# Kernel tuning notes

Measured on AMD Instinct MI355X. Metric: run time of the kernel, lower is better.

The kernel has to match this reference:

```python
import jax, jax.numpy as jnp
import numpy as np

NEG_INF = jnp.float32(-1e30)


def setup_inputs() -> dict:
    key = jax.random.key(0)
    k1, k2, k3, k4 = jax.random.split(key, 4)
    B, L1, L2, H = 64, 1024, 1024, 128
    x = jax.random.normal(k1, (B, L1, H), dtype=jnp.float32)
    y = jax.random.normal(k2, (B, L2, H), dtype=jnp.float32)
    y_mask = jax.random.uniform(k3, (B, L2)) < 0.2
    W = jax.random.normal(k4, (H, H), dtype=jnp.float32) * (1.0 / np.sqrt(H))
    b = jnp.zeros((H,), dtype=jnp.float32)
    return {"x": x, "y": y, "y_mask": y_mask, "W": W, "b": b}


def reference(x, y, y_mask, W, b):
    # shared linear + relu projections (torch Linear: x @ W.T + b)
    x_proj = jax.nn.relu(jnp.einsum("bld,hd->blh", x, W) + b)  # [B, L1, H]
    y_proj = jax.nn.relu(jnp.einsum("bld,hd->blh", y, W) + b)  # [B, L2, H]
    # unscaled cross-attention scores
    scores = jnp.einsum("bih,bjh->bij", x_proj, y_proj)  # [B, L1, L2]
    scores = jnp.where(y_mask[:, None, :], NEG_INF, scores)
    alpha = jax.nn.softmax(scores, axis=-1)  # [B, L1, L2]
    # weighted sum over original (unprojected) y
    matched_seq = jnp.einsum("bij,bjh->bih", alpha, y)  # [B, L1, H]
    return matched_seq
```

## Files before the change

### kernel.cpp

```cpp
#include <hip/hip_runtime.h>
#include <hip/hip_bf16.h>


typedef __attribute__((ext_vector_type(8))) short    s8v;
typedef __attribute__((ext_vector_type(8))) _Float16 h8v;
typedef __attribute__((ext_vector_type(4))) _Float16 h4v;
typedef __attribute__((ext_vector_type(4))) float    f4v;

#define BDIM 256

__device__ __forceinline__ f4v mfma_bf16(s8v a, s8v b, f4v c) {
    return __builtin_amdgcn_mfma_f32_16x16x32_bf16(a, b, c, 0, 0, 0);
}
__device__ __forceinline__ f4v mfma_f16(h8v a, h8v b, f4v c) {
    return __builtin_amdgcn_mfma_f32_16x16x32_f16(a, b, c, 0, 0, 0);
}
__device__ __forceinline__ void tsplit(float v, short& hi, short& lo) {
    unsigned b = __builtin_bit_cast(unsigned, v);
    unsigned hb = b & 0xFFFF0000u;
    float res = v - __builtin_bit_cast(float, hb);
    hi = (short)(hb >> 16);
    lo = (short)(__builtin_bit_cast(unsigned, res) >> 16);
}

typedef const __attribute__((address_space(1))) unsigned int gu32;
typedef __attribute__((address_space(3))) unsigned int lu32;
__device__ __forceinline__ void gld_lds16(const void* g, void* l) {
    __builtin_amdgcn_global_load_lds((gu32*)g, (lu32*)l, 16, 0, 0);
}

__global__ __launch_bounds__(1024) void prep_kernel(
    const unsigned int* __restrict__ mraw, unsigned char* __restrict__ nm,
    const float* __restrict__ W, short* __restrict__ Whsw, short* __restrict__ Wlsw)
{
    if (blockIdx.x == 1) {
        for (int idx = threadIdx.x; idx < 16384; idx += 1024) {
            int r = idx >> 7, c = idx & 127;
            short hi, lo; tsplit(W[idx], hi, lo);
            int cs = (((c >> 3) ^ (r & 15)) << 3) | (c & 7);
            Whsw[r * 128 + cs] = hi;
            Wlsw[r * 128 + cs] = lo;
        }
        return;
    }
    __shared__ unsigned int sOrAll, sOrOdd;
    if (threadIdx.x == 0) { sOrAll = 0u; sOrOdd = 0u; }
    __syncthreads();
    unsigned int oa = 0u, oo = 0u;
    for (int i = threadIdx.x; i < 16384; i += 1024) {
        unsigned int v = mraw[i];
        oa |= v;
        if (i & 1) oo |= v;
    }
    atomicOr(&sOrAll, oa);
    atomicOr(&sOrOdd, oo);
    __syncthreads();
    const unsigned int orv = sOrAll, oro = sOrOdd;
    int mode;
    if (orv <= 1u)                       mode = (orv == 1u && oro == 0u) ? 3 : 0;
    else if ((orv & 0xFEFEFEFEu) == 0u)  mode = 1;
    else if ((orv & 0x0000FFFFu) == 0u)  mode = 0;
    else                                 mode = 2;
    const unsigned char*  b8  = (const unsigned char*)mraw;
    const unsigned short* b16 = (const unsigned short*)mraw;
    for (int j = threadIdx.x; j < 65536; j += 1024) {
        unsigned int v;
        if (mode == 0)      v = mraw[j];
        else if (mode == 1) v = b8[j];
        else if (mode == 2) v = b16[j];
        else                v = mraw[2 * j] | mraw[2 * j + 1];
        nm[j] = v ? 1 : 0;
    }
}

__global__ __launch_bounds__(BDIM, 4) void proj_kernel(
    const float* __restrict__ X, const float* __restrict__ Y,
    const short* __restrict__ Whsw, const short* __restrict__ Wlsw,
    const float* __restrict__ bias,
    _Float16* __restrict__ XPf, _Float16* __restrict__ YPsw,
    _Float16* __restrict__ YTsw)
{
    __shared__ short sW[2][64][128];

    const int gid = blockIdx.x;
    const float* src; int local;
    if (gid < 1024) { src = X; local = gid; }
    else            { src = Y; local = gid - 1024; }
    const int row0 = (local >> 1) * 128, h0 = (local & 1) * 64;
    const int t = threadIdx.x, w = t >> 6, lane = t & 63, c = lane & 15, q = lane >> 4;

    {
        const short* g0 = Whsw + h0 * 128;
        const short* g1 = Wlsw + h0 * 128;
        short* l0 = &sW[0][0][0];
        short* l1 = &sW[1][0][0];
        for (int i = 0; i < 4; ++i) {
            int off = (t + i * BDIM) * 8;
            *(s8v*)(l0 + off) = *(const s8v*)(g0 + off);
            *(s8v*)(l1 + off) = *(const s8v*)(g1 + off);
        }
    }

    f4v rawA[2][4], rawB[2][4];
#pragma unroll
    for (int set = 0; set < 2; ++set) {
        const float* xr = src + (size_t)(row0 + w * 32 + set * 16 + c) * 128;
#pragma unroll
        for (int ks = 0; ks < 4; ++ks) {
            rawA[set][ks] = *(const f4v*)&xr[ks * 32 + q * 8];
            rawB[set][ks] = *(const f4v*)&xr[ks * 32 + q * 8 + 4];
        }
    }
    __syncthreads();

    f4v zero = {0.f, 0.f, 0.f, 0.f};
#pragma unroll
    for (int set = 0; set < 2; ++set) {
        s8v ah[4], al[4];
#pragma unroll
        for (int ks = 0; ks < 4; ++ks) {
            for (int k = 0; k < 4; ++k) {
                short hh, ll;
                tsplit(rawA[set][ks][k], hh, ll); ah[ks][k] = hh;     al[ks][k] = ll;
                tsplit(rawB[set][ks][k], hh, ll); ah[ks][4 + k] = hh; al[ks][4 + k] = ll;
            }
        }
        f4v acc[4];
        for (int n = 0; n < 4; ++n) acc[n] = zero;
#pragma unroll
        for (int ks = 0; ks < 4; ++ks) {
            s8v bh[4], bl[4];
            for (int nt = 0; nt < 4; ++nt) {
                int cs = (((ks * 4 + q) ^ c) << 3);
                bh[nt] = *(const s8v*)&sW[0][nt * 16 + c][cs];
                bl[nt] = *(const s8v*)&sW[1][nt * 16 + c][cs];
            }
            for (int nt = 0; nt < 4; ++nt) {
                acc[nt] = mfma_bf16(ah[ks], bh[nt], acc[nt]);
                acc[nt] = mfma_bf16(al[ks], bh[nt], acc[nt]);
                acc[nt] = mfma_bf16(ah[ks], bl[nt], acc[nt]);
            }
        }
        for (int nt = 0; nt < 4; ++nt) {
            float bv = bias[h0 + nt * 16 + c];
            for (int r = 0; r < 4; ++r) {
                float v = fmaxf(acc[nt][r] + bv, 0.0f);
                int grow = row0 + w * 32 + set * 16 + q * 4 + r;
                int h = h0 + nt * 16 + c;
                if (gid < 1024) {
                    XPf[(size_t)grow * 128 + h] = (_Float16)v;
                } else {
                    int jt = (grow >> 6) & 15, jr = grow & 63;
                    int chunk = (h >> 3) ^ (jr & 7);
                    size_t off = (size_t)((grow >> 10) * 16 + jt) * 8192
                                 + jr * 128 + chunk * 8 + (h & 7);
                    YPsw[off] = (_Float16)v;
                }
            }
        }
    }

    if (gid >= 1024 && h0 == 0) {
        __syncthreads();
        _Float16* sT = (_Float16*)&sW[0][0][0];
#pragma unroll
        for (int set = 0; set < 2; ++set) {
            int row = w * 32 + set * 16 + c;
            int tile = row >> 6, j6 = row & 63;
            int jlo = j6 & 7, jhb = (j6 >> 3);
#pragma unroll
            for (int ks = 0; ks < 4; ++ks) {
                for (int k = 0; k < 4; ++k) {
                    int h = ks * 32 + q * 8 + k;
                    sT[tile * 8192 + h * 64 + (((jhb ^ (h & 7)) << 3) | jlo)] =
                        (_Float16)rawA[set][ks][k];
                    int h2 = h + 4;
                    sT[tile * 8192 + h2 * 64 + (((jhb ^ (h2 & 7)) << 3) | jlo)] =
                        (_Float16)rawB[set][ks][k];
                }
            }
        }
        __syncthreads();
        _Float16* dst = YTsw + (size_t)(row0 >> 6) * 8192;
        for (int i = 0; i < 8; ++i) {
            int idx = t + i * BDIM;
            *(h8v*)(dst + idx * 8) = *(const h8v*)(sT + idx * 8);
        }
    }
}

__global__ __launch_bounds__(512, 4) void attn_kernel(
    const _Float16* __restrict__ YPsw, const _Float16* __restrict__ YTsw,
    const unsigned char* __restrict__ nmask,
    const _Float16* __restrict__ XPf, float* __restrict__ out)
{
    __shared__ _Float16 sTile[2][16384];
    __shared__ _Float16 sP[128 * 64];

    const int id = blockIdx.x;
    const int xcd = id & 7, rest = id >> 3;
    const int ibase = (rest & 7) * 128;
    const int b = xcd + 8 * (rest >> 3);
    const int t = threadIdx.x, wave = t >> 6, lane = t & 63;
    const int c = lane & 15, q = lane >> 4;
    const int mrow = b * 1024;

    h8v afrag[4];
    {
        const _Float16* xr = XPf + (size_t)(mrow + ibase + wave * 16 + c) * 128;
        for (int ks = 0; ks < 4; ++ks)
            afrag[ks] = *(const h8v*)&xr[ks * 32 + q * 8];
    }

    const char* gYP = (const char*)(YPsw + (size_t)b * 16 * 8192);
    const char* gYT = (const char*)(YTsw + (size_t)b * 16 * 8192);
    const int soff = wave * 1024 + lane * 16;

    {
        char* lp = (char*)&sTile[0][0]    + wave * 1024;
        char* lt = (char*)&sTile[0][8192] + wave * 1024;
        for (int i = 0; i < 2; ++i) {
            gld_lds16(gYP + soff + i * 8192, lp + i * 8192);
            gld_lds16(gYT + soff + i * 8192, lt + i * 8192);
        }
    }

    unsigned mw[4];
    for (int nt = 0; nt < 4; ++nt)
        mw[nt] = *(const unsigned*)(nmask + mrow + nt * 16 + q * 4);

    f4v zero = {0.f, 0.f, 0.f, 0.f};
    float m_s = -INFINITY, l_s = 0.f;
    f4v o[8];
    for (int h = 0; h < 8; ++h) o[h] = zero;

    const int srcbase = (lane & 48) + ((lane >> 4) << 2);
    const int cb = q ^ (c & 7);
    const int prow = (wave * 16 + c) * 64;
    const int pwofs = (q & 1) * 4;

    __syncthreads();

    int cur = 0;
    for (int jt = 0; jt < 16; ++jt) {
        const int jbase = jt * 64;
        const int nx = cur ^ 1;

        if (jt < 15) {
            const char* gp = gYP + (size_t)(jt + 1) * 16384;
            const char* gt = gYT + (size_t)(jt + 1) * 16384;
            char* lp = (char*)&sTile[nx][0]    + wave * 1024;
            char* lt = (char*)&sTile[nx][8192] + wave * 1024;
            for (int i = 0; i < 2; ++i) {
                gld_lds16(gp + soff + i * 8192, lp + i * 8192);
                gld_lds16(gt + soff + i * 8192, lt + i * 8192);
            }
        }

        f4v s[4];
        __builtin_amdgcn_s_setprio(1);
        for (int nt = 0; nt < 4; ++nt) {
            const _Float16* rp = &sTile[cur][0] + (nt * 16 + c) * 128;
            h8v f0 = *(const h8v*)(rp + ((cb ^ 0) << 3));
            h8v f1 = *(const h8v*)(rp + ((cb ^ 4) << 3));
            h8v f2 = *(const h8v*)(rp + ((cb ^ 8) << 3));
            h8v f3 = *(const h8v*)(rp + ((cb ^ 12) << 3));
            f4v acc = zero;
            acc = mfma_f16(f0, afrag[0], acc);
            acc = mfma_f16(f1, afrag[1], acc);
            acc = mfma_f16(f2, afrag[2], acc);
            acc = mfma_f16(f3, afrag[3], acc);
            s[nt] = acc;
        }
        __builtin_amdgcn_s_setprio(0);

        for (int nt = 0; nt < 4; ++nt)
            for (int r = 0; r < 4; ++r)
                if ((mw[nt] >> (r * 8)) & 0xFFu) s[nt][r] = -1e30f;

        float mx = fmaxf(
            fmaxf(fmaxf(fmaxf(s[0][0], s[0][1]), fmaxf(s[0][2], s[0][3])),
                  fmaxf(fmaxf(s[1][0], s[1][1]), fmaxf(s[1][2], s[1][3]))),
            fmaxf(fmaxf(fmaxf(s[2][0], s[2][1]), fmaxf(s[2][2], s[2][3])),
                  fmaxf(fmaxf(s[3][0], s[3][1]), fmaxf(s[3][2], s[3][3]))));
        mx = fmaxf(mx, __shfl_xor(mx, 16, 64));
        mx = fmaxf(mx, __shfl_xor(mx, 32, 64));
        float mnew = fmaxf(m_s, mx);
        float alpha = __expf(m_s - mnew);
        m_s = mnew;

        float rsum = 0.f;
        for (int nt = 0; nt < 4; ++nt) {
            h4v ph4;
            for (int r = 0; r < 4; ++r) {
                float p = ((mw[nt] >> (r * 8)) & 0xFFu) ? 0.f
                          : __expf(s[nt][r] - mnew);
                _Float16 ph = (_Float16)p;
                rsum += (float)ph;
                ph4[r] = ph;
            }
            int ck = (2 * nt + (q >> 1)) ^ (c & 7);
            *(h4v*)&sP[prow + ck * 8 + pwofs] = ph4;
        }
        rsum += __shfl_xor(rsum, 16, 64);
        rsum += __shfl_xor(rsum, 32, 64);
        l_s = l_s * alpha + rsum;

        if (jt < 15) {
            const int jn = jbase + 64;
            for (int nt = 0; nt < 4; ++nt)
                mw[nt] = *(const unsigned*)(nmask + mrow + jn + nt * 16 + q * 4);
        }

        float aD0 = __shfl(alpha, srcbase + 0, 64);
        float aD1 = __shfl(alpha, srcbase + 1, 64);
        float aD2 = __shfl(alpha, srcbase + 2, 64);
        float aD3 = __shfl(alpha, srcbase + 3, 64);
        for (int h = 0; h < 8; ++h) {
            o[h][0] *= aD0; o[h][1] *= aD1; o[h][2] *= aD2; o[h][3] *= aD3;
        }

        __builtin_amdgcn_s_setprio(1);
        for (int k2 = 0; k2 < 2; ++k2) {
            h8v a = *(const h8v*)&sP[prow + (((k2 << 2) + q) ^ (c & 7)) * 8];
            const _Float16* yt = &sTile[cur][8192];
            for (int hb = 0; hb < 8; ++hb) {
                h8v bb = *(const h8v*)(yt + (hb * 16 + c) * 64
                                       + ((((k2 << 2) + q) ^ (c & 7)) << 3));
                o[hb] = mfma_f16(a, bb, o[hb]);
            }
        }
        __builtin_amdgcn_s_setprio(0);

        __syncthreads();
        cur = nx;
    }

    float lD[4];
    lD[0] = __shfl(l_s, srcbase + 0, 64);
    lD[1] = __shfl(l_s, srcbase + 1, 64);
    lD[2] = __shfl(l_s, srcbase + 2, 64);
    lD[3] = __shfl(l_s, srcbase + 3, 64);
    for (int h = 0; h < 8; ++h) {
        for (int r = 0; r < 4; ++r) {
            float v = o[h][r] / lD[r];
            out[(size_t)(mrow + ibase + wave * 16 + q * 4 + r) * 128 + h * 16 + c] = v;
        }
    }
}

extern "C" void kernel_launch(void* const* d_in, const int* in_sizes, int n_in,
                              void* d_out, int out_size, void* d_ws, size_t ws_size,
                              hipStream_t stream) {
    const float* x    = (const float*)d_in[0];
    const float* y    = (const float*)d_in[1];
    const unsigned int* mraw = (const unsigned int*)d_in[2];
    const float* W    = (const float*)d_in[3];
    const float* bias = (const float*)d_in[4];
    float* out = (float*)d_out;

    unsigned char* nmask = (unsigned char*)d_ws;
    short* Whsw = (short*)((char*)d_ws + 65536);
    short* Wlsw = Whsw + 16384;
    _Float16* XPf = (_Float16*)(Wlsw + 16384);
    _Float16* YPsw = XPf + (size_t)64 * 1024 * 128;
    _Float16* YTsw = YPsw + (size_t)64 * 1024 * 128;

    prep_kernel<<<2, 1024, 0, stream>>>(mraw, nmask, W, Whsw, Wlsw);
    proj_kernel<<<2048, BDIM, 0, stream>>>(x, y, Whsw, Wlsw, bias, XPf, YPsw, YTsw);
    attn_kernel<<<512, 512, 0, stream>>>(YPsw, YTsw, nmask, XPf, out);
}
```

Measured before the change: 215.7 us.

## Stage projection outputs through LDS for vector stores and distribute mask conversion

Projection results are buffered in shared memory with the required swizzle and then written to global memory as 16-byte vectors, replacing scattered 2-byte stores. The mask normalization, previously done serially by a single block in the prep kernel, moves into the first 64 projection blocks, with the prep kernel only publishing the OR summaries. This adds extra barriers and LDS traffic in the projection kernel and some load imbalance on the first blocks.

```diff
diff --git a/kernel.cpp b/kernel.cpp
--- a/kernel.cpp
+++ b/kernel.cpp
@@ -30,7 +30,7 @@
 }
 
 __global__ __launch_bounds__(1024) void prep_kernel(
-    const unsigned int* __restrict__ mraw, unsigned char* __restrict__ nm,
+    const unsigned int* __restrict__ mraw, unsigned int* __restrict__ orw,
     const float* __restrict__ W, short* __restrict__ Whsw, short* __restrict__ Wlsw)
 {
     if (blockIdx.x == 1) {
@@ -55,28 +55,14 @@
     atomicOr(&sOrAll, oa);
     atomicOr(&sOrOdd, oo);
     __syncthreads();
-    const unsigned int orv = sOrAll, oro = sOrOdd;
-    int mode;
-    if (orv <= 1u)                       mode = (orv == 1u && oro == 0u) ? 3 : 0;
-    else if ((orv & 0xFEFEFEFEu) == 0u)  mode = 1;
-    else if ((orv & 0x0000FFFFu) == 0u)  mode = 0;
-    else                                 mode = 2;
-    const unsigned char*  b8  = (const unsigned char*)mraw;
-    const unsigned short* b16 = (const unsigned short*)mraw;
-    for (int j = threadIdx.x; j < 65536; j += 1024) {
-        unsigned int v;
-        if (mode == 0)      v = mraw[j];
-        else if (mode == 1) v = b8[j];
-        else if (mode == 2) v = b16[j];
-        else                v = mraw[2 * j] | mraw[2 * j + 1];
-        nm[j] = v ? 1 : 0;
-    }
+    if (threadIdx.x == 0) { orw[0] = sOrAll; orw[1] = sOrOdd; }
 }
 
 __global__ __launch_bounds__(BDIM, 4) void proj_kernel(
     const float* __restrict__ X, const float* __restrict__ Y,
     const short* __restrict__ Whsw, const short* __restrict__ Wlsw,
-    const float* __restrict__ bias,
+    const float* __restrict__ bias, const unsigned int* __restrict__ orw,
+    const unsigned int* __restrict__ mraw, unsigned char* __restrict__ nm,
     _Float16* __restrict__ XPf, _Float16* __restrict__ YPsw,
     _Float16* __restrict__ YTsw)
 {
@@ -84,8 +70,9 @@
 
     const int gid = blockIdx.x;
     const float* src; int local;
-    if (gid < 1024) { src = X; local = gid; }
-    else            { src = Y; local = gid - 1024; }
+    const bool isY = (gid >= 1024);
+    if (!isY) { src = X; local = gid; }
+    else      { src = Y; local = gid - 1024; }
     const int row0 = (local >> 1) * 128, h0 = (local & 1) * 64;
     const int t = threadIdx.x, w = t >> 6, lane = t & 63, c = lane & 15, q = lane >> 4;
 
@@ -114,6 +101,7 @@
     __syncthreads();
 
     f4v zero = {0.f, 0.f, 0.f, 0.f};
+    h4v res[2][4];
 #pragma unroll
     for (int set = 0; set < 2; ++set) {
         s8v ah[4], al[4];
@@ -143,24 +131,42 @@
         }
         for (int nt = 0; nt < 4; ++nt) {
             float bv = bias[h0 + nt * 16 + c];
+            for (int r = 0; r < 4; ++r)
+                res[set][nt][r] = (_Float16)fmaxf(acc[nt][r] + bv, 0.0f);
+        }
+    }
+
+    __syncthreads();
+    _Float16* sE = (_Float16*)&sW[0][0][0];
+#pragma unroll
+    for (int set = 0; set < 2; ++set)
+        for (int nt = 0; nt < 4; ++nt)
             for (int r = 0; r < 4; ++r) {
-                float v = fmaxf(acc[nt][r] + bv, 0.0f);
-                int grow = row0 + w * 32 + set * 16 + q * 4 + r;
-                int h = h0 + nt * 16 + c;
-                if (gid < 1024) {
-                    XPf[(size_t)grow * 128 + h] = (_Float16)v;
-                } else {
-                    int jt = (grow >> 6) & 15, jr = grow & 63;
-                    int chunk = (h >> 3) ^ (jr & 7);
-                    size_t off = (size_t)((grow >> 10) * 16 + jt) * 8192
-                                 + jr * 128 + chunk * 8 + (h & 7);
-                    YPsw[off] = (_Float16)v;
-                }
-            }
-        }
-    }
-
-    if (gid >= 1024 && h0 == 0) {
+                int lr = w * 32 + set * 16 + q * 4 + r;
+                int col;
+                if (isY) col = (((2 * nt + (c >> 3)) ^ (lr & 7)) << 3) | (c & 7);
+                else     col = nt * 16 + c;
+                sE[lr * 72 + col] = res[set][nt][r];
+            }
+    __syncthreads();
+    if (!isY) {
+        for (int i = 0; i < 4; ++i) {
+            int idx = t + i * BDIM;
+            int lr = idx >> 3, pos = (idx & 7) * 8;
+            *(h8v*)(XPf + (size_t)(row0 + lr) * 128 + h0 + pos) =
+                *(const h8v*)(sE + lr * 72 + pos);
+        }
+    } else {
+        for (int i = 0; i < 4; ++i) {
+            int idx = t + i * BDIM;
+            int lr = idx >> 3, pos = (idx & 7) * 8;
+            *(h8v*)(YPsw + (size_t)((row0 + lr) >> 6) * 8192
+                    + (size_t)(lr & 63) * 128 + h0 + pos) =
+                *(const h8v*)(sE + lr * 72 + pos);
+        }
+    }
+
+    if (isY && h0 == 0) {
         __syncthreads();
         _Float16* sT = (_Float16*)&sW[0][0][0];
 #pragma unroll
@@ -185,6 +191,27 @@
         for (int i = 0; i < 8; ++i) {
             int idx = t + i * BDIM;
             *(h8v*)(dst + idx * 8) = *(const h8v*)(sT + idx * 8);
+        }
+    }
+
+    if (gid < 64) {
+        const unsigned orv = orw[0], oro = orw[1];
+        int mode;
+        if (orv <= 1u)                       mode = (orv == 1u && oro == 0u) ? 3 : 0;
+        else if ((orv & 0xFEFEFEFEu) == 0u)  mode = 1;
+        else if ((orv & 0x0000FFFFu) == 0u)  mode = 0;
+        else                                 mode = 2;
+        const unsigned char*  b8  = (const unsigned char*)mraw;
+        const unsigned short* b16 = (const unsigned short*)mraw;
+        const int base = gid * 1024;
+        for (int i = t; i < 1024; i += BDIM) {
+            int j = base + i;
+            unsigned v;
+            if (mode == 0)      v = mraw[j];
+            else if (mode == 1) v = b8[j];
+            else if (mode == 2) v = b16[j];
+            else                v = mraw[2 * j] | mraw[2 * j + 1];
+            nm[j] = v ? 1 : 0;
         }
     }
 }
@@ -362,11 +389,13 @@
     unsigned char* nmask = (unsigned char*)d_ws;
     short* Whsw = (short*)((char*)d_ws + 65536);
     short* Wlsw = Whsw + 16384;
-    _Float16* XPf = (_Float16*)(Wlsw + 16384);
+    unsigned int* orw = (unsigned int*)((char*)d_ws + 131072);
+    _Float16* XPf = (_Float16*)((char*)d_ws + 135168);
     _Float16* YPsw = XPf + (size_t)64 * 1024 * 128;
     _Float16* YTsw = YPsw + (size_t)64 * 1024 * 128;
 
-    prep_kernel<<<2, 1024, 0, stream>>>(mraw, nmask, W, Whsw, Wlsw);
-    proj_kernel<<<2048, BDIM, 0, stream>>>(x, y, Whsw, Wlsw, bias, XPf, YPsw, YTsw);
+    prep_kernel<<<2, 1024, 0, stream>>>(mraw, orw, W, Whsw, Wlsw);
+    proj_kernel<<<2048, BDIM, 0, stream>>>(x, y, Whsw, Wlsw, bias, orw,
+                                           mraw, nmask, XPf, YPsw, YTsw);
     attn_kernel<<<512, 512, 0, stream>>>(YPsw, YTsw, nmask, XPf, out);
 }
```

After: 199.7 us. 1.08x faster.
